# Performance work log

Measured on AMD Instinct MI355X. Metric: run time of the kernel, lower is better.

## Reference

```python
import jax, jax.numpy as jnp
import numpy as np

N_NODES = 50000
N_EDGES = 800000
IN_DIM = 8
EDGE_DIM = 4
HIDDEN = 16
OUT_DIM = 1


def _lin_init(key, fan_in, fan_out):
    kw, kb = jax.random.split(key)
    bound = 1.0 / np.sqrt(fan_in)
    W = jax.random.uniform(kw, (fan_in, fan_out), minval=-bound, maxval=bound, dtype=jnp.float32)
    b = jax.random.uniform(kb, (fan_out,), minval=-bound, maxval=bound, dtype=jnp.float32)
    return W, b


def setup_inputs() -> dict:
    key = jax.random.key(0)
    ks = jax.random.split(key, 16)
    x = jax.random.normal(ks[0], (N_NODES, IN_DIM), dtype=jnp.float32)
    edge_index = jax.random.randint(ks[1], (2, N_EDGES), 0, N_NODES, dtype=jnp.int32)
    edge_attr = jax.random.normal(ks[2], (N_EDGES, EDGE_DIM), dtype=jnp.float32)

    inp = {"x": x, "edge_index": edge_index, "edge_attr": edge_attr}
    in_dims = [IN_DIM, HIDDEN]
    for i in range(2):
        d_in = in_dims[i]
        W1, b1 = _lin_init(ks[3 + 4 * i], EDGE_DIM, HIDDEN)
        W2, b2 = _lin_init(ks[4 + 4 * i], HIDDEN, d_in * HIDDEN)
        root = jax.random.uniform(ks[5 + 4 * i], (d_in, HIDDEN), minval=-1.0 / np.sqrt(d_in), maxval=1.0 / np.sqrt(d_in), dtype=jnp.float32)
        bias = jnp.zeros((HIDDEN,), dtype=jnp.float32)
        inp[f"eW1_{i}"] = W1; inp[f"eb1_{i}"] = b1
        inp[f"eW2_{i}"] = W2; inp[f"eb2_{i}"] = b2
        inp[f"root_{i}"] = root; inp[f"bias_{i}"] = bias
    mW1, mb1 = _lin_init(ks[11], HIDDEN, HIDDEN)
    mW2, mb2 = _lin_init(ks[12], HIDDEN, OUT_DIM)
    inp["mW1"] = mW1; inp["mb1"] = mb1; inp["mW2"] = mW2; inp["mb2"] = mb2
    return inp


def _nnconv(x, src, dst, edge_attr, eW1, eb1, eW2, eb2, root, bias):
    # edge MLP -> per-edge weight matrix [E, d_in, HIDDEN]
    h = jax.nn.silu(edge_attr @ eW1 + eb1)
    Wedge = (h @ eW2 + eb2).reshape(edge_attr.shape[0], x.shape[1], HIDDEN)
    # gather source features, per-edge matmul, scatter-mean to targets
    msg = jnp.einsum('ei,eio->eo', x[src], Wedge)  # [E, HIDDEN]
    agg = jax.ops.segment_sum(msg, dst, num_segments=N_NODES)
    cnt = jax.ops.segment_sum(jnp.ones((msg.shape[0],), dtype=msg.dtype), dst, num_segments=N_NODES)
    agg = agg / jnp.maximum(cnt, 1.0)[:, None]
    return x @ root + agg + bias


def reference(x, edge_index, edge_attr,
              eW1_0, eb1_0, eW2_0, eb2_0, root_0, bias_0,
              eW1_1, eb1_1, eW2_1, eb2_1, root_1, bias_1,
              mW1, mb1, mW2, mb2):
    src, dst = edge_index[0], edge_index[1]
    x = jax.nn.relu(_nnconv(x, src, dst, edge_attr, eW1_0, eb1_0, eW2_0, eb2_0, root_0, bias_0))
    x = jax.nn.relu(_nnconv(x, src, dst, edge_attr, eW1_1, eb1_1, eW2_1, eb2_1, root_1, bias_1))
    out = jax.nn.sigmoid(jax.nn.silu(x @ mW1 + mb1) @ mW2 + mb2)
    return out
```

## Files before the change

kernel.cpp:

```cpp
#include <hip/hip_runtime.h>
#include <hip/hip_fp16.h>

#define NN 50000
#define NE 800000
#define NBUCK 196

__device__ __forceinline__ float sigm(float v) { return 1.0f / (1.0f + __expf(-v)); }


__global__ void sort_count(const int* __restrict__ ei,
                           int* __restrict__ cntA, int* __restrict__ cntB)
{
    __shared__ int hA[NBUCK], hB[NBUCK];
    int t = threadIdx.x;
    for (int i = t; i < NBUCK; i += 256) { hA[i] = 0; hB[i] = 0; }
    __syncthreads();
    int base = blockIdx.x * 2048;
#pragma unroll
    for (int r = 0; r < 8; ++r) {
        int idx = base + r * 256 + t;
        if (idx < NE) {
            int s = ei[idx], d = ei[NE + idx];
            atomicAdd(&hB[s >> 8], 1);
            atomicAdd(&hA[d >> 8], 1);
        }
    }
    __syncthreads();
    for (int i = t; i < NBUCK; i += 256) {
        if (hA[i]) atomicAdd(&cntA[i], hA[i]);
        if (hB[i]) atomicAdd(&cntB[i], hB[i]);
    }
}

__global__ void sort_scan(const int* __restrict__ cntA, const int* __restrict__ cntB,
                          int* __restrict__ baseA, int* __restrict__ baseB,
                          int* __restrict__ curA,  int* __restrict__ curB)
{
    __shared__ int a[256], b[256];
    int t = threadIdx.x;
    a[t] = (t < NBUCK) ? cntA[t] : 0;
    b[t] = (t < NBUCK) ? cntB[t] : 0;
    __syncthreads();
#pragma unroll
    for (int dd = 1; dd < 256; dd <<= 1) {
        int av = (t >= dd) ? a[t - dd] : 0;
        int bv = (t >= dd) ? b[t - dd] : 0;
        __syncthreads();
        a[t] += av; b[t] += bv;
        __syncthreads();
    }
    int exA = (t > 0) ? a[t - 1] : 0;
    int exB = (t > 0) ? b[t - 1] : 0;
    if (t < NBUCK) { baseA[t] = exA; curA[t] = exA; baseB[t] = exB; curB[t] = exB; }
    if (t == 255)  { baseA[NBUCK] = a[255]; baseB[NBUCK] = b[255]; }
}

__global__ __launch_bounds__(256) void sort_scatterA(const int* __restrict__ ei,
                                                     int* __restrict__ curA,
                                                     unsigned long long* __restrict__ recA)
{
    __shared__ int lcnt[NBUCK];
    __shared__ int lofs[NBUCK];
    int t = threadIdx.x;
    for (int i = t; i < NBUCK; i += 256) lcnt[i] = 0;
    __syncthreads();
    int base = blockIdx.x * 2048;
#pragma unroll
    for (int r = 0; r < 8; ++r) {
        int e = base + r * 256 + t;
        if (e < NE) atomicAdd(&lcnt[ei[NE + e] >> 8], 1);
    }
    __syncthreads();
    for (int i = t; i < NBUCK; i += 256)
        lofs[i] = lcnt[i] ? atomicAdd(&curA[i], lcnt[i]) : 0;
    __syncthreads();
#pragma unroll
    for (int r = 0; r < 8; ++r) {
        int e = base + r * 256 + t;
        if (e < NE) {
            int s = ei[e], d = ei[NE + e];
            int p = atomicAdd(&lofs[d >> 8], 1);
            recA[p] = ((unsigned long long)(unsigned)(d & 255) << 36)
                    | ((unsigned long long)(unsigned)s << 20)
                    | (unsigned long long)(unsigned)e;
        }
    }
}

__global__ __launch_bounds__(256) void sort_localA(const unsigned long long* __restrict__ recA,
                                                   const int* __restrict__ baseA,
                                                   int* __restrict__ off_all,
                                                   unsigned long long* __restrict__ dlist)
{
    __shared__ int c[256];
    __shared__ int live[256];
    int t = threadIdx.x;
    int b = blockIdx.x;
    int lo = baseA[b], hi = baseA[b + 1];
    c[t] = 0;
    __syncthreads();
    for (int i = lo + t; i < hi; i += 256)
        atomicAdd(&c[(int)(recA[i] >> 36) & 255], 1);
    __syncthreads();
#pragma unroll
    for (int dd = 1; dd < 256; dd <<= 1) {
        int v = (t >= dd) ? c[t - dd] : 0;
        __syncthreads();
        c[t] += v;
        __syncthreads();
    }
    int ex = (t > 0) ? c[t - 1] : 0;
    int d = (b << 8) + t;
    if (d <= NN) off_all[d] = lo + ex;
    live[t] = lo + ex;
    __syncthreads();
    for (int i = lo + t; i < hi; i += 256) {
        unsigned long long rec = recA[i];
        int pos = atomicAdd(&live[(int)(rec >> 36) & 255], 1);
        dlist[pos] = rec & 0xFFFFFFFFFull;
    }
}

__global__ __launch_bounds__(256) void sort_scatterB(const unsigned long long* __restrict__ dlist,
                                                     int* __restrict__ curB,
                                                     unsigned long long* __restrict__ recB)
{
    __shared__ int lcnt[NBUCK];
    __shared__ int lofs[NBUCK];
    __shared__ unsigned long long vS[2048];
    int t = threadIdx.x;
    for (int i = t; i < NBUCK; i += 256) lcnt[i] = 0;
    __syncthreads();
    int base = blockIdx.x * 2048;
#pragma unroll
    for (int r = 0; r < 8; ++r) {
        int dp = base + r * 256 + t;
        int li = r * 256 + t;
        if (dp < NE) {
            unsigned long long v = dlist[dp];
            vS[li] = v;
            atomicAdd(&lcnt[(int)(v >> 28)], 1);
        }
    }
    __syncthreads();
    for (int i = t; i < NBUCK; i += 256)
        lofs[i] = lcnt[i] ? atomicAdd(&curB[i], lcnt[i]) : 0;
    __syncthreads();
#pragma unroll
    for (int r = 0; r < 8; ++r) {
        int dp = base + r * 256 + t;
        int li = r * 256 + t;
        if (dp < NE) {
            unsigned long long v = vS[li];
            int s = (int)((v >> 20) & 0xFFFFu);
            int p = atomicAdd(&lofs[s >> 8], 1);
            recB[p] = ((unsigned long long)(unsigned)(s & 255) << 40)
                    | ((unsigned long long)(unsigned)dp << 20)
                    | (v & 0xFFFFFull);
        }
    }
}

__global__ __launch_bounds__(256) void sort_localB(const unsigned long long* __restrict__ recB,
                                                   const int* __restrict__ baseB,
                                                   const float4* __restrict__ ea4,
                                                   int* __restrict__ off_all,
                                                   unsigned* __restrict__ sperm32,
                                                   float4* __restrict__ ea_perm)
{
    __shared__ int c[256];
    __shared__ int live[256];
    int t = threadIdx.x;
    int b = blockIdx.x;
    int lo = baseB[b], hi = baseB[b + 1];
    c[t] = 0;
    __syncthreads();
    for (int i = lo + t; i < hi; i += 256)
        atomicAdd(&c[(int)(recB[i] >> 40) & 255], 1);
    __syncthreads();
#pragma unroll
    for (int dd = 1; dd < 256; dd <<= 1) {
        int v = (t >= dd) ? c[t - dd] : 0;
        __syncthreads();
        c[t] += v;
        __syncthreads();
    }
    int ex = (t > 0) ? c[t - 1] : 0;
    int s = (b << 8) + t;
    if (s <= NN) off_all[NN + s] = NE + lo + ex;
    live[t] = lo + ex;
    __syncthreads();
    for (int i = lo + t; i < hi; i += 256) {
        unsigned long long rec = recB[i];
        int k = (int)(rec >> 40) & 255;
        int pos = atomicAdd(&live[k], 1);
        unsigned sl = (unsigned)(((b << 8) + k) & 15);
        unsigned dp = (unsigned)((rec >> 20) & 0xFFFFFu);
        sperm32[pos] = (sl << 20) | dp;
        ea_perm[pos] = ea4[rec & 0xFFFFFull];
    }
}

template<int DIN>
__global__ __launch_bounds__(256) void edge_fusedG(
        const float* __restrict__ xin,
        const unsigned* __restrict__ sperm32,
        const float4* __restrict__ ea_perm,
        const float* __restrict__ eW1,
        const float* __restrict__ eb1,
        const float* __restrict__ eW2,
        const float* __restrict__ eb2,
        const int*   __restrict__ off_all,
        __half* __restrict__ msgbuf)
{
    constexpr int MROW = 260;
    constexpr int W2B  = DIN * 16 * 20 * 4;
    constexpr int SMB  = 16 * MROW * 4 + 256 * 4;
    constexpr int UNIB = (W2B > SMB) ? W2B : SMB;
    __shared__ __align__(16) char uni[UNIB];
    float* w2L   = (float*)uni;
    float* smemM = (float*)uni;
    int*   sdp   = (int*)(uni + 16 * MROW * 4);
    __shared__ __align__(16) float4 G4[16 * 69];
    __shared__ __align__(16) float4 xbL[16 * 5];
    __shared__ __align__(16) float  xL[16 * DIN];
    __shared__ __align__(16) float  b2L[DIN * 16];
    __shared__ __align__(16) float4 w1t[16];
    __shared__ __align__(16) float  b1s[16];

    int tid = threadIdx.x;
    int nb  = blockIdx.x * 16;
    if (tid < 16) {
        w1t[tid] = make_float4(eW1[tid], eW1[16 + tid], eW1[32 + tid], eW1[48 + tid]);
        b1s[tid] = eb1[tid];
    }
    for (int t = tid; t < 16 * DIN * 16; t += 256) {
        int k = t / (DIN * 16);
        int rem = t - k * DIN * 16;
        int i = rem >> 4, o = rem & 15;
        w2L[(i * 16 + k) * 20 + o] = eW2[t];
    }
    for (int t = tid; t < DIN * 16; t += 256) b2L[t] = eb2[t];
    for (int t = tid; t < 16 * DIN; t += 256) xL[t] = xin[(size_t)nb * DIN + t];
    __syncthreads();

    {
        int nl = tid >> 4, k = tid & 15;
        const float* xrow = xL + nl * DIN;
#pragma unroll
        for (int ob = 0; ob < 4; ++ob) {
            float4 a4 = make_float4(0.f, 0.f, 0.f, 0.f);
#pragma unroll
            for (int i = 0; i < DIN; ++i) {
                const float4 w = *((const float4*)(w2L + (i * 16 + k) * 20) + ob);
                a4.x += xrow[i] * w.x; a4.y += xrow[i] * w.y;
                a4.z += xrow[i] * w.z; a4.w += xrow[i] * w.w;
            }
            G4[nl * 69 + ob * 17 + k] = a4;
        }
        if (k < 4) {
            int ob = k;
            const float4* b2v = (const float4*)b2L;
            float4 a4 = make_float4(0.f, 0.f, 0.f, 0.f);
#pragma unroll
            for (int i = 0; i < DIN; ++i) {
                float4 b = b2v[i * 4 + ob];
                a4.x += xrow[i] * b.x; a4.y += xrow[i] * b.y;
                a4.z += xrow[i] * b.z; a4.w += xrow[i] * b.w;
            }
            xbL[nl * 5 + ob] = a4;
        }
    }
    __syncthreads();

    int eBeg = off_all[NN + nb] - NE;
    int eEnd = off_all[NN + nb + 16] - NE;
    for (int cb = eBeg; cb < eEnd; cb += 256) {
        int pos = cb + tid;
        bool valid = pos < eEnd;
        unsigned pk = valid ? sperm32[pos] : 0u;
        int dp = (int)(pk & 0xFFFFFu);
        int sl = (int)(pk >> 20);
        float4 a = valid ? ea_perm[pos] : make_float4(0.f, 0.f, 0.f, 0.f);

        float h[16];
#pragma unroll
        for (int j = 0; j < 16; ++j) {
            float4 w = w1t[j];
            float p = b1s[j] + a.x * w.x + a.y * w.y + a.z * w.z + a.w * w.w;
            h[j] = p * sigm(p);
        }
        float4 acc[4];
#pragma unroll
        for (int ob = 0; ob < 4; ++ob) acc[ob] = xbL[sl * 5 + ob];
#pragma unroll
        for (int k = 0; k < 16; ++k) {
            float hk = h[k];
#pragma unroll
            for (int ob = 0; ob < 4; ++ob) {
                float4 g = G4[sl * 69 + ob * 17 + k];
                acc[ob].x += hk * g.x; acc[ob].y += hk * g.y;
                acc[ob].z += hk * g.z; acc[ob].w += hk * g.w;
            }
        }
        sdp[tid] = valid ? dp : -1;
#pragma unroll
        for (int ob = 0; ob < 4; ++ob) {
            smemM[(ob * 4 + 0) * MROW + tid] = acc[ob].x;
            smemM[(ob * 4 + 1) * MROW + tid] = acc[ob].y;
            smemM[(ob * 4 + 2) * MROW + tid] = acc[ob].z;
            smemM[(ob * 4 + 3) * MROW + tid] = acc[ob].w;
        }
        __syncthreads();
#pragma unroll
        for (int r = 0; r < 8; ++r) {
            int le = r * 32 + (tid >> 3);
            int p  = tid & 7;
            int d2 = sdp[le];
            float v0 = smemM[(2 * p)     * MROW + le];
            float v1 = smemM[(2 * p + 1) * MROW + le];
            if (d2 >= 0) {
                __half2 hv = __floats2half2_rn(v0, v1);
                *((__half2*)(msgbuf + (size_t)d2 * 16) + p) = hv;
            }
        }
        __syncthreads();
    }
}

__device__ __forceinline__ float gather_msg16(const __half* __restrict__ msgbuf,
                                              int s0, int e0, int tid)
{
    int half = (tid >> 3) & 1;
    int p    = tid & 7;
    float ax = 0.f, ay = 0.f;
    for (int j = s0 + half; j < e0; j += 2) {
        __half2 hv = *((const __half2*)(msgbuf + (size_t)j * 16) + p);
        float2 f = __half22float2(hv);
        ax += f.x; ay += f.y;
    }
    ax += __shfl_xor(ax, 8, 16);
    ay += __shfl_xor(ay, 8, 16);
    int ch = tid & 15;
    float vx = __shfl(ax, ch >> 1, 16);
    float vy = __shfl(ay, ch >> 1, 16);
    return (ch & 1) ? vy : vx;
}

__global__ __launch_bounds__(256) void gather_L0(
        const float* __restrict__ xin,
        const float* __restrict__ root,
        const float* __restrict__ bias,
        const int*   __restrict__ off_all,
        const __half* __restrict__ msgbuf,
        float* __restrict__ x1)
{
    __shared__ __align__(16) float rootL[8 * 16];
    __shared__ __align__(16) float biasL[16];
    int tid = threadIdx.x;
    if (tid < 128) rootL[tid] = root[tid];
    if (tid < 16) biasL[tid] = bias[tid];
    __syncthreads();

    int ch = tid & 15;
    int n  = blockIdx.x * 16 + (tid >> 4);
    int s0 = off_all[n], e0 = off_all[n + 1];

    float acc = gather_msg16(msgbuf, s0, e0, tid);
    float v = acc / fmaxf((float)(e0 - s0), 1.0f) + biasL[ch];
#pragma unroll
    for (int i = 0; i < 8; ++i)
        v += xin[(size_t)n * 8 + i] * rootL[i * 16 + ch];
    x1[(size_t)n * 16 + ch] = fmaxf(v, 0.f);
}

__global__ __launch_bounds__(256) void gather_final(
        const float* __restrict__ x1,
        const float* __restrict__ root,
        const float* __restrict__ bias,
        const int*   __restrict__ off_all,
        const __half* __restrict__ msgbuf,
        const float* __restrict__ mW1,
        const float* __restrict__ mb1,
        const float* __restrict__ mW2,
        const float* __restrict__ mb2,
        float* __restrict__ out)
{
    __shared__ __align__(16) float rootL[256];
    __shared__ __align__(16) float biasL[16];
    __shared__ __align__(16) float w1m[256];
    __shared__ __align__(16) float b1m[16];
    __shared__ __align__(16) float w2m[16];
    __shared__ float b2m;
    int tid = threadIdx.x;
    rootL[tid] = root[tid];
    w1m[tid] = mW1[tid];
    if (tid < 16) { biasL[tid] = bias[tid]; b1m[tid] = mb1[tid]; w2m[tid] = mW2[tid]; }
    if (tid == 0) b2m = mb2[0];
    __syncthreads();

    int ch = tid & 15;
    int n  = blockIdx.x * 16 + (tid >> 4);
    int s0 = off_all[n], e0 = off_all[n + 1];

    float acc = gather_msg16(msgbuf, s0, e0, tid);
    float v = acc / fmaxf((float)(e0 - s0), 1.0f) + biasL[ch];
#pragma unroll
    for (int i = 0; i < 16; ++i)
        v += x1[(size_t)n * 16 + i] * rootL[i * 16 + ch];
    v = fmaxf(v, 0.f);

    float z = b1m[ch];
#pragma unroll
    for (int o = 0; o < 16; ++o) {
        float vo = __shfl(v, o, 16);
        z += vo * w1m[o * 16 + ch];
    }
    float ss = z * sigm(z) * w2m[ch];
#pragma unroll
    for (int off = 8; off; off >>= 1) ss += __shfl_xor(ss, off, 16);
    if (ch == 0) out[n] = sigm(ss + b2m);
}

extern "C" void kernel_launch(void* const* d_in, const int* in_sizes, int n_in,
                              void* d_out, int out_size, void* d_ws, size_t ws_size,
                              hipStream_t stream) {
    const float* x     = (const float*)d_in[0];
    const int*   ei    = (const int*)  d_in[1];
    const float* ea    = (const float*)d_in[2];
    const float* eW1_0 = (const float*)d_in[3];
    const float* eb1_0 = (const float*)d_in[4];
    const float* eW2_0 = (const float*)d_in[5];
    const float* eb2_0 = (const float*)d_in[6];
    const float* root0 = (const float*)d_in[7];
    const float* bias0 = (const float*)d_in[8];
    const float* eW1_1 = (const float*)d_in[9];
    const float* eb1_1 = (const float*)d_in[10];
    const float* eW2_1 = (const float*)d_in[11];
    const float* eb2_1 = (const float*)d_in[12];
    const float* root1 = (const float*)d_in[13];
    const float* bias1 = (const float*)d_in[14];
    const float* mW1   = (const float*)d_in[15];
    const float* mb1   = (const float*)d_in[16];
    const float* mW2   = (const float*)d_in[17];
    const float* mb2   = (const float*)d_in[18];
    float* out = (float*)d_out;

    const int GG  = NN / 16;
    const int SBK = (NE + 2047) / 2048;

    int* W = (int*)d_ws;
    int* off_all = W;
    int* cntA    = W + 100004;
    int* cntB    = W + 100260;
    int* baseA   = W + 100516;
    int* baseB   = W + 100716;
    int* curA    = W + 100916;
    int* curB    = W + 101172;
    unsigned* sperm32 = (unsigned*)(W + 101440);
    float4* ea_perm   = (float4*)(W + 901440);
    float*  x1        = (float*)(W + 4101440);
    __half* msgbuf    = (__half*)(W + 4901440);
    unsigned long long* recA  = (unsigned long long*)(W + 4901440);
    unsigned long long* dlist = (unsigned long long*)(W + 6501440);
    unsigned long long* recB  = (unsigned long long*)(W + 8101440);

    hipMemsetAsync(cntA, 0, 512 * sizeof(int), stream);
    sort_count   <<<SBK,   256, 0, stream>>>(ei, cntA, cntB);
    sort_scan    <<<1,     256, 0, stream>>>(cntA, cntB, baseA, baseB, curA, curB);
    sort_scatterA<<<SBK,   256, 0, stream>>>(ei, curA, recA);
    sort_localA  <<<NBUCK, 256, 0, stream>>>(recA, baseA, off_all, dlist);
    sort_scatterB<<<SBK,   256, 0, stream>>>(dlist, curB, recB);
    sort_localB  <<<NBUCK, 256, 0, stream>>>(recB, baseB, (const float4*)ea,
                                             off_all, sperm32, ea_perm);

    edge_fusedG<8><<<GG, 256, 0, stream>>>(x, sperm32, ea_perm, eW1_0, eb1_0,
                                           eW2_0, eb2_0, off_all, msgbuf);
    gather_L0<<<GG, 256, 0, stream>>>(x, root0, bias0, off_all, msgbuf, x1);

    edge_fusedG<16><<<GG, 256, 0, stream>>>(x1, sperm32, ea_perm, eW1_1, eb1_1,
                                            eW2_1, eb2_1, off_all, msgbuf);
    gather_final<<<GG, 256, 0, stream>>>(x1, root1, bias1, off_all, msgbuf,
                                         mW1, mb1, mW2, mb2, out);
}
```

Baseline: 300.9 us.

## Double sort bucket count and repack edge-weight smem layout for float4 reads

Bucket width drops from 256 to 128 nodes, so there are 392 buckets. The local sort kernels now launch twice as many smaller blocks, which fills more of the GPU, and the scan kernel is widened to 512 threads to match. In the edge kernel, the second-layer weights are re-laid out in shared memory so each float4 read is contiguous without padding, which also shrinks that buffer. The message write-out loop now runs only over valid edge rows. In exchange, half the threads sit idle during the per-bucket scan, and the workspace offsets and memset size all had to be recomputed.

Result: faster. 289.4 us (-3.8%).

```diff
diff --git a/kernel.cpp b/kernel.cpp
--- a/kernel.cpp
+++ b/kernel.cpp
@@ -3,7 +3,7 @@
 
 #define NN 50000
 #define NE 800000
-#define NBUCK 196
+#define NBUCK 392
 
 __device__ __forceinline__ float sigm(float v) { return 1.0f / (1.0f + __expf(-v)); }
 
@@ -21,8 +21,8 @@
         int idx = base + r * 256 + t;
         if (idx < NE) {
             int s = ei[idx], d = ei[NE + idx];
-            atomicAdd(&hB[s >> 8], 1);
-            atomicAdd(&hA[d >> 8], 1);
+            atomicAdd(&hB[s >> 7], 1);
+            atomicAdd(&hA[d >> 7], 1);
         }
     }
     __syncthreads();
@@ -36,13 +36,13 @@
                           int* __restrict__ baseA, int* __restrict__ baseB,
                           int* __restrict__ curA,  int* __restrict__ curB)
 {
-    __shared__ int a[256], b[256];
+    __shared__ int a[512], b[512];
     int t = threadIdx.x;
     a[t] = (t < NBUCK) ? cntA[t] : 0;
     b[t] = (t < NBUCK) ? cntB[t] : 0;
     __syncthreads();
 #pragma unroll
-    for (int dd = 1; dd < 256; dd <<= 1) {
+    for (int dd = 1; dd < 512; dd <<= 1) {
         int av = (t >= dd) ? a[t - dd] : 0;
         int bv = (t >= dd) ? b[t - dd] : 0;
         __syncthreads();
@@ -52,7 +52,7 @@
     int exA = (t > 0) ? a[t - 1] : 0;
     int exB = (t > 0) ? b[t - 1] : 0;
     if (t < NBUCK) { baseA[t] = exA; curA[t] = exA; baseB[t] = exB; curB[t] = exB; }
-    if (t == 255)  { baseA[NBUCK] = a[255]; baseB[NBUCK] = b[255]; }
+    if (t == 511)  { baseA[NBUCK] = a[511]; baseB[NBUCK] = b[511]; }
 }
 
 __global__ __launch_bounds__(256) void sort_scatterA(const int* __restrict__ ei,
@@ -68,7 +68,7 @@
 #pragma unroll
     for (int r = 0; r < 8; ++r) {
         int e = base + r * 256 + t;
-        if (e < NE) atomicAdd(&lcnt[ei[NE + e] >> 8], 1);
+        if (e < NE) atomicAdd(&lcnt[ei[NE + e] >> 7], 1);
     }
     __syncthreads();
     for (int i = t; i < NBUCK; i += 256)
@@ -79,8 +79,8 @@
         int e = base + r * 256 + t;
         if (e < NE) {
             int s = ei[e], d = ei[NE + e];
-            int p = atomicAdd(&lofs[d >> 8], 1);
-            recA[p] = ((unsigned long long)(unsigned)(d & 255) << 36)
+            int p = atomicAdd(&lofs[d >> 7], 1);
+            recA[p] = ((unsigned long long)(unsigned)(d & 127) << 36)
                     | ((unsigned long long)(unsigned)s << 20)
                     | (unsigned long long)(unsigned)e;
         }
@@ -92,31 +92,33 @@
                                                    int* __restrict__ off_all,
                                                    unsigned long long* __restrict__ dlist)
 {
-    __shared__ int c[256];
-    __shared__ int live[256];
+    __shared__ int c[128];
+    __shared__ int live[128];
     int t = threadIdx.x;
     int b = blockIdx.x;
     int lo = baseA[b], hi = baseA[b + 1];
-    c[t] = 0;
+    if (t < 128) c[t] = 0;
     __syncthreads();
     for (int i = lo + t; i < hi; i += 256)
-        atomicAdd(&c[(int)(recA[i] >> 36) & 255], 1);
-    __syncthreads();
-#pragma unroll
-    for (int dd = 1; dd < 256; dd <<= 1) {
-        int v = (t >= dd) ? c[t - dd] : 0;
-        __syncthreads();
-        c[t] += v;
-        __syncthreads();
-    }
-    int ex = (t > 0) ? c[t - 1] : 0;
-    int d = (b << 8) + t;
-    if (d <= NN) off_all[d] = lo + ex;
-    live[t] = lo + ex;
+        atomicAdd(&c[(int)(recA[i] >> 36) & 127], 1);
+    __syncthreads();
+#pragma unroll
+    for (int dd = 1; dd < 128; dd <<= 1) {
+        int v = (t >= dd && t < 128) ? c[t - dd] : 0;
+        __syncthreads();
+        if (t < 128) c[t] += v;
+        __syncthreads();
+    }
+    if (t < 128) {
+        int ex = (t > 0) ? c[t - 1] : 0;
+        int d = (b << 7) + t;
+        if (d <= NN) off_all[d] = lo + ex;
+        live[t] = lo + ex;
+    }
     __syncthreads();
     for (int i = lo + t; i < hi; i += 256) {
         unsigned long long rec = recA[i];
-        int pos = atomicAdd(&live[(int)(rec >> 36) & 255], 1);
+        int pos = atomicAdd(&live[(int)(rec >> 36) & 127], 1);
         dlist[pos] = rec & 0xFFFFFFFFFull;
     }
 }
@@ -139,7 +141,7 @@
         if (dp < NE) {
             unsigned long long v = dlist[dp];
             vS[li] = v;
-            atomicAdd(&lcnt[(int)(v >> 28)], 1);
+            atomicAdd(&lcnt[(int)(v >> 27) & 511], 1);
         }
     }
     __syncthreads();
@@ -153,8 +155,8 @@
         if (dp < NE) {
             unsigned long long v = vS[li];
             int s = (int)((v >> 20) & 0xFFFFu);
-            int p = atomicAdd(&lofs[s >> 8], 1);
-            recB[p] = ((unsigned long long)(unsigned)(s & 255) << 40)
+            int p = atomicAdd(&lofs[s >> 7], 1);
+            recB[p] = ((unsigned long long)(unsigned)(s & 127) << 40)
                     | ((unsigned long long)(unsigned)dp << 20)
                     | (v & 0xFFFFFull);
         }
@@ -168,33 +170,35 @@
                                                    unsigned* __restrict__ sperm32,
                                                    float4* __restrict__ ea_perm)
 {
-    __shared__ int c[256];
-    __shared__ int live[256];
+    __shared__ int c[128];
+    __shared__ int live[128];
     int t = threadIdx.x;
     int b = blockIdx.x;
     int lo = baseB[b], hi = baseB[b + 1];
-    c[t] = 0;
+    if (t < 128) c[t] = 0;
     __syncthreads();
     for (int i = lo + t; i < hi; i += 256)
-        atomicAdd(&c[(int)(recB[i] >> 40) & 255], 1);
-    __syncthreads();
-#pragma unroll
-    for (int dd = 1; dd < 256; dd <<= 1) {
-        int v = (t >= dd) ? c[t - dd] : 0;
-        __syncthreads();
-        c[t] += v;
-        __syncthreads();
-    }
-    int ex = (t > 0) ? c[t - 1] : 0;
-    int s = (b << 8) + t;
-    if (s <= NN) off_all[NN + s] = NE + lo + ex;
-    live[t] = lo + ex;
+        atomicAdd(&c[(int)(recB[i] >> 40) & 127], 1);
+    __syncthreads();
+#pragma unroll
+    for (int dd = 1; dd < 128; dd <<= 1) {
+        int v = (t >= dd && t < 128) ? c[t - dd] : 0;
+        __syncthreads();
+        if (t < 128) c[t] += v;
+        __syncthreads();
+    }
+    if (t < 128) {
+        int ex = (t > 0) ? c[t - 1] : 0;
+        int s = (b << 7) + t;
+        if (s <= NN) off_all[NN + s] = NE + lo + ex;
+        live[t] = lo + ex;
+    }
     __syncthreads();
     for (int i = lo + t; i < hi; i += 256) {
         unsigned long long rec = recB[i];
-        int k = (int)(rec >> 40) & 255;
+        int k = (int)(rec >> 40) & 127;
         int pos = atomicAdd(&live[k], 1);
-        unsigned sl = (unsigned)(((b << 8) + k) & 15);
+        unsigned sl = (unsigned)(k & 15);
         unsigned dp = (unsigned)((rec >> 20) & 0xFFFFFu);
         sperm32[pos] = (sl << 20) | dp;
         ea_perm[pos] = ea4[rec & 0xFFFFFull];
@@ -214,13 +218,13 @@
         __half* __restrict__ msgbuf)
 {
     constexpr int MROW = 260;
-    constexpr int W2B  = DIN * 16 * 20 * 4;
+    constexpr int W2B  = DIN * 64 * 16;
     constexpr int SMB  = 16 * MROW * 4 + 256 * 4;
     constexpr int UNIB = (W2B > SMB) ? W2B : SMB;
     __shared__ __align__(16) char uni[UNIB];
-    float* w2L   = (float*)uni;
-    float* smemM = (float*)uni;
-    int*   sdp   = (int*)(uni + 16 * MROW * 4);
+    float*  w2Lf  = (float*)uni;
+    float*  smemM = (float*)uni;
+    int*    sdp   = (int*)(uni + 16 * MROW * 4);
     __shared__ __align__(16) float4 G4[16 * 69];
     __shared__ __align__(16) float4 xbL[16 * 5];
     __shared__ __align__(16) float  xL[16 * DIN];
@@ -238,7 +242,7 @@
         int k = t / (DIN * 16);
         int rem = t - k * DIN * 16;
         int i = rem >> 4, o = rem & 15;
-        w2L[(i * 16 + k) * 20 + o] = eW2[t];
+        w2Lf[((((o >> 2) * DIN + i) * 16) + k) * 4 + (o & 3)] = eW2[t];
     }
     for (int t = tid; t < DIN * 16; t += 256) b2L[t] = eb2[t];
     for (int t = tid; t < 16 * DIN; t += 256) xL[t] = xin[(size_t)nb * DIN + t];
@@ -247,12 +251,13 @@
     {
         int nl = tid >> 4, k = tid & 15;
         const float* xrow = xL + nl * DIN;
+        const float4* w2L4 = (const float4*)uni;
 #pragma unroll
         for (int ob = 0; ob < 4; ++ob) {
             float4 a4 = make_float4(0.f, 0.f, 0.f, 0.f);
 #pragma unroll
             for (int i = 0; i < DIN; ++i) {
-                const float4 w = *((const float4*)(w2L + (i * 16 + k) * 20) + ob);
+                float4 w = w2L4[(ob * DIN + i) * 16 + k];
                 a4.x += xrow[i] * w.x; a4.y += xrow[i] * w.y;
                 a4.z += xrow[i] * w.z; a4.w += xrow[i] * w.w;
             }
@@ -312,8 +317,9 @@
             smemM[(ob * 4 + 3) * MROW + tid] = acc[ob].w;
         }
         __syncthreads();
-#pragma unroll
-        for (int r = 0; r < 8; ++r) {
+        int nvalid = eEnd - cb; if (nvalid > 256) nvalid = 256;
+        int nr = (nvalid + 31) >> 5;
+        for (int r = 0; r < nr; ++r) {
             int le = r * 32 + (tid >> 3);
             int p  = tid & 7;
             int d2 = sdp[le];
@@ -452,22 +458,22 @@
     int* W = (int*)d_ws;
     int* off_all = W;
     int* cntA    = W + 100004;
-    int* cntB    = W + 100260;
-    int* baseA   = W + 100516;
-    int* baseB   = W + 100716;
-    int* curA    = W + 100916;
-    int* curB    = W + 101172;
-    unsigned* sperm32 = (unsigned*)(W + 101440);
-    float4* ea_perm   = (float4*)(W + 901440);
-    float*  x1        = (float*)(W + 4101440);
-    __half* msgbuf    = (__half*)(W + 4901440);
-    unsigned long long* recA  = (unsigned long long*)(W + 4901440);
-    unsigned long long* dlist = (unsigned long long*)(W + 6501440);
-    unsigned long long* recB  = (unsigned long long*)(W + 8101440);
-
-    hipMemsetAsync(cntA, 0, 512 * sizeof(int), stream);
+    int* cntB    = W + 100400;
+    int* baseA   = W + 100800;
+    int* baseB   = W + 101200;
+    int* curA    = W + 101600;
+    int* curB    = W + 102000;
+    unsigned* sperm32 = (unsigned*)(W + 102400);
+    float4* ea_perm   = (float4*)(W + 902400);
+    float*  x1        = (float*)(W + 4102400);
+    __half* msgbuf    = (__half*)(W + 4902400);
+    unsigned long long* recA  = (unsigned long long*)(W + 4902400);
+    unsigned long long* dlist = (unsigned long long*)(W + 6502400);
+    unsigned long long* recB  = (unsigned long long*)(W + 8102400);
+
+    hipMemsetAsync(cntA, 0, 2 * 396 * sizeof(int), stream);
     sort_count   <<<SBK,   256, 0, stream>>>(ei, cntA, cntB);
-    sort_scan    <<<1,     256, 0, stream>>>(cntA, cntB, baseA, baseB, curA, curB);
+    sort_scan    <<<1,     512, 0, stream>>>(cntA, cntB, baseA, baseB, curA, curB);
     sort_scatterA<<<SBK,   256, 0, stream>>>(ei, curA, recA);
     sort_localA  <<<NBUCK, 256, 0, stream>>>(recA, baseA, off_all, dlist);
     sort_scatterB<<<SBK,   256, 0, stream>>>(dlist, curB, recB);
```
